# Optimization experiments

Measured on AMD Instinct MI355X. Metric: run time of the kernel, lower is better.

The kernel has to match this reference:

```python
import jax, jax.numpy as jnp
import numpy as np

N_USER = 150_000
M_ITEM = 30_000
N_NODES = N_USER + M_ITEM
D = 64                      # embedding_dim
N_LAYERS = 3                # gcn_layer_number
E = 600_000                 # user-item interactions (symmetric nnz = 2E)
B = 1024
NUM_RATE, NUM_GENRE, NUM_DIR, NUM_ACT = 6, 25, 2186, 8030
NUM_GENDER, NUM_AGE, NUM_OCC, NUM_ZIP = 2, 7, 21, 3402
H1, H2 = 64, 64             # first/second fc hidden dims
FC1_IN = D * 10


def setup_inputs() -> dict:
    key = jax.random.key(0)
    ks = jax.random.split(key, 24)
    # aux features: 0/1 values are valid indices for every categorical field
    aux_info = jax.random.randint(ks[0], (B, 10246), 0, 2, dtype=jnp.int32)
    user_ids = jax.random.randint(ks[1], (B,), 0, N_USER, dtype=jnp.int32)
    item_ids = jax.random.randint(ks[2], (B,), 0, M_ITEM, dtype=jnp.int32)
    # bipartite graph: random interactions, symmetric normalized adjacency
    u = jax.random.randint(ks[3], (E,), 0, N_USER, dtype=jnp.int32)
    i = jax.random.randint(ks[4], (E,), 0, M_ITEM, dtype=jnp.int32) + N_USER
    graph_row = jnp.concatenate([u, i])
    graph_col = jnpph = jnp.concatenate([i, u]) if False else jnp.concatenate([i, u])
    deg = jax.ops.segment_sum(jnp.ones((2 * E,), jnp.float32), graph_row, num_segments=N_NODES)
    dinv = jnp.where(deg > 0, jax.lax.rsqrt(jnp.maximum(deg, 1.0)), 0.0)
    graph_val = dinv[graph_row] * dinv[graph_col]
    s = 0.1
    nrm = lambda k, shp: (jax.random.normal(k, shp, jnp.float32) * s)
    return {
        "aux_info": aux_info, "user_ids": user_ids, "item_ids": item_ids,
        "graph_row": graph_row, "graph_col": graph_col, "graph_val": graph_val,
        "rate_tab": nrm(ks[5], (NUM_RATE, D)),
        "genre_W": nrm(ks[6], (NUM_GENRE, D)),
        "director_W": nrm(ks[7], (NUM_DIR, D)),
        "actor_W": nrm(ks[8], (NUM_ACT, D)),
        "gender_tab": nrm(ks[9], (NUM_GENDER, D)),
        "age_tab": nrm(ks[10], (NUM_AGE, D)),
        "occ_tab": nrm(ks[11], (NUM_OCC, D)),
        "area_tab": nrm(ks[12], (NUM_ZIP, D)),
        "user_rel": nrm(ks[13], (N_USER, D)),
        "item_rel": nrm(ks[14], (M_ITEM, D)),
        "fc1_W": nrm(ks[15], (FC1_IN, H1)), "fc1_b": jnp.zeros((H1,), jnp.float32),
        "fc2_W": nrm(ks[16], (H1, H2)), "fc2_b": jnp.zeros((H2,), jnp.float32),
        "out_W": nrm(ks[17], (H2, 1)), "out_b": jnp.zeros((1,), jnp.float32),
    }


def _lightgcn(user_rel, item_rel, row, col, val):
    # LightGCN: repeated SpMM D^-1/2 A D^-1/2 @ emb, mean over layer outputs
    emb = jnp.concatenate([user_rel, item_rel], axis=0)      # [N, D]
    acc = emb
    for _ in range(N_LAYERS):
        emb = jax.ops.segment_sum(val[:, None] * emb[col], row, num_segments=N_NODES)
        acc = acc + emb
    light = acc / (N_LAYERS + 1)
    return light[:N_USER], light[N_USER:]


def _multi_hot(idx_int, W):
    x = idx_int.astype(jnp.float32)
    return (x @ W) / jnp.sum(x, axis=1, keepdims=True)


def reference(aux_info, user_ids, item_ids, graph_row, graph_col, graph_val,
              rate_tab, genre_W, director_W, actor_W,
              gender_tab, age_tab, occ_tab, area_tab,
              user_rel, item_rel,
              fc1_W, fc1_b, fc2_W, fc2_b, out_W, out_b):
    rate_idx = aux_info[:, 0]
    genre_idx = aux_info[:, 1:26]
    director_idx = aux_info[:, 26:2212]
    actor_idx = aux_info[:, 2212:10242]
    gender_idx = aux_info[:, 10242]
    age_idx = aux_info[:, 10243]
    occ_idx = aux_info[:, 10244]
    area_idx = aux_info[:, 10245]

    item_emb = jnp.concatenate([
        rate_tab[rate_idx],
        _multi_hot(genre_idx, genre_W),
        _multi_hot(director_idx, director_W),
        _multi_hot(actor_idx, actor_W),
    ], axis=1)                                               # [B, 4D]
    user_emb = jnp.concatenate([
        gender_tab[gender_idx], age_tab[age_idx],
        occ_tab[occ_idx], area_tab[area_idx],
    ], axis=1)                                               # [B, 4D]

    all_users, all_items = _lightgcn(user_rel, item_rel, graph_row, graph_col, graph_val)
    X = jnp.concatenate([item_emb, user_emb,
                         all_users[user_ids], all_items[item_ids]], axis=1)  # [B, 10D]
    X = jax.nn.relu(X @ fc1_W + fc1_b)
    X = jax.nn.relu(X @ fc2_W + fc2_b)
    return X @ out_W + out_b                                 # [B, 1]
```

## Files before the change

kernel.cpp:

```cpp
#include <hip/hip_runtime.h>
#include <hip/hip_bf16.h>
#include <hip/hip_fp16.h>

#define N_USER 150000
#define M_ITEM 30000
#define N_NODES 180000
#define E2 1200000
#define BATCH 1024
#define AUX_W 10246
#define KP_G 32
#define KP_D 2208
#define KP_A 8064
#define NBKT 265
#define WT_BLKS 2576
#define BCNT_BLKS 293
#define MH_BLKS 672
#define CVT_BLKS 5625

typedef __attribute__((ext_vector_type(8))) short short8;
typedef __attribute__((ext_vector_type(8))) unsigned short ushort8_t;
typedef __attribute__((ext_vector_type(4))) float f32x4;

__device__ __forceinline__ int bucket_of(int r) {
    return r < N_USER ? (r >> 10) : 147 + ((r - N_USER) >> 8);
}

__device__ __forceinline__ int detect_f32(const void* probe) {
    float v = __bfloat162float(((const __hip_bfloat16*)probe)[threadIdx.x & 63]);
    unsigned long long m = __ballot(!(fabsf(v) < 1000.0f));
    return __popcll(m) > 8;
}

struct CvtSeg { const void* src; float* dst; int n; int blk0; };
struct CvtBatch { CvtSeg seg[16]; };

__global__ void __launch_bounds__(256) k_prep(CvtBatch cb, int cvtBlks,
                                              const void* Wg, const void* Wd, const void* Wa,
                                              unsigned short* WtG, unsigned short* WtD, unsigned short* WtA,
                                              const int* __restrict__ grow, int* __restrict__ bucket_tot,
                                              const void* probe) {
    int blk = blockIdx.x, tid = threadIdx.x;
    if (blk < BCNT_BLKS) {
        __shared__ int h[NBKT];
        for (int i = tid; i < NBKT; i += 256) h[i] = 0;
        __syncthreads();
        int idx0 = blk * 4096;
        #pragma unroll
        for (int k = 0; k < 16; ++k) {
            int i = idx0 + k * 256 + tid;
            if (i < E2) atomicAdd(&h[bucket_of(grow[i])], 1);
        }
        __syncthreads();
        for (int i = tid; i < NBKT; i += 256) if (h[i]) atomicAdd(&bucket_tot[i], h[i]);
        return;
    }
    if (blk < BCNT_BLKS + cvtBlks) {
        int isf32 = detect_f32(probe);
        int cblk = blk - BCNT_BLKS;
        int si = 0;
        #pragma unroll
        for (int i = 0; i < 16; ++i) if (cblk >= cb.seg[i].blk0) si = i;
        const CvtSeg sg = cb.seg[si];
        int i = (cblk - sg.blk0) * 256 + tid;
        if (i >= sg.n) return;
        if (isf32) sg.dst[i] = ((const float*)sg.src)[i];
        else       sg.dst[i] = __bfloat162float(((const __hip_bfloat16*)sg.src)[i]);
        return;
    }
    {
        int isf32 = detect_f32(probe);
        int t = (blk - BCNT_BLKS - cvtBlks) * 256 + tid;
        if (t >= (KP_G + KP_D + KP_A) * 64) return;
        int kp = t >> 6, n = t & 63;
        int k, K; const void* src; unsigned short* dst;
        if (kp < KP_G)              { k = kp;               K = 25;   src = Wg; dst = WtG; }
        else if (kp < KP_G + KP_D)  { k = kp - KP_G;        K = 2186; src = Wd; dst = WtD; }
        else                        { k = kp - KP_G - KP_D; K = 8030; src = Wa; dst = WtA; }
        unsigned short v = 0;
        if (k < K) {
            if (isf32) {
                __hip_bfloat16 h = __float2bfloat16(((const float*)src)[(size_t)k * 64 + n]);
                v = *(unsigned short*)&h;
            } else {
                v = ((const unsigned short*)src)[(size_t)k * 64 + n];
            }
        }
        dst[(((size_t)(k >> 5) * 64 + n) * 4 + ((k >> 3) & 3)) * 8 + (k & 7)] = v;
    }
}

__global__ void __launch_bounds__(512) k_bscan(const int* __restrict__ bucket_tot,
                                               int* __restrict__ bucket_base,
                                               int* __restrict__ bucketcur) {
    __shared__ int s[512];
    int tid = threadIdx.x;
    s[tid] = (tid < NBKT) ? bucket_tot[tid] : 0;
    __syncthreads();
    for (int off = 1; off < 512; off <<= 1) {
        int v = (tid >= off) ? s[tid - off] : 0;
        __syncthreads();
        s[tid] += v;
        __syncthreads();
    }
    int excl = tid ? s[tid - 1] : 0;
    bucket_base[tid] = excl;
    if (tid < NBKT) bucketcur[tid] = excl;
}

__device__ void mhgemm_body(int blk, const int* __restrict__ aux,
                            const unsigned short* __restrict__ WtG,
                            const unsigned short* __restrict__ WtD,
                            const unsigned short* __restrict__ WtA,
                            float* __restrict__ Xmh, float* __restrict__ cntf) {
    int seg, rb, k0, klen, Kseg, auxoff;
    const unsigned short* Wt;
    if (blk < 16)       { seg = 0; rb = blk;                      k0 = 0;              klen = 25;                  Kseg = 25;   auxoff = 1;    Wt = WtG; }
    else if (blk < 160) { int t = blk - 16;  seg = 1; rb = t & 15; k0 = (t >> 4) * 256; klen = min(256, 2186 - k0); Kseg = 2186; auxoff = 26;   Wt = WtD; }
    else                { int t = blk - 160; seg = 2; rb = t & 15; k0 = (t >> 4) * 256; klen = min(256, 8030 - k0); Kseg = 8030; auxoff = 2212; Wt = WtA; }
    int lane = threadIdx.x & 63, wave = threadIdx.x >> 6;
    int m = lane & 15, quad = lane >> 4;
    int row = rb * 64 + wave * 16 + m;
    const int* arow = aux + (size_t)row * AUX_W + auxoff;

    f32x4 acc0 = {0.f,0.f,0.f,0.f}, acc1 = acc0, acc2 = acc0, acc3 = acc0;
    int isum = 0;
    int nchunk = (klen + 31) >> 5;
    int pa[8], na[8];
    auto lda = [&](int kci, int (&A)[8]) {
        int kb = k0 + kci * 32 + quad * 8;
        if (kb + 8 <= Kseg) {
            #pragma unroll
            for (int j = 0; j < 8; ++j) A[j] = arow[kb + j];
        } else {
            #pragma unroll
            for (int j = 0; j < 8; ++j) A[j] = (kb + j < Kseg) ? arow[kb + j] : 0;
        }
    };
    lda(0, pa);
    for (int kci = 0; kci < nchunk; ++kci) {
        if (kci + 1 < nchunk) lda(kci + 1, na);
        union { unsigned u[4]; short8 s; } af;
        af.u[0] = (unsigned)pa[0] * 16256u + (unsigned)pa[1] * 0x3F800000u;
        af.u[1] = (unsigned)pa[2] * 16256u + (unsigned)pa[3] * 0x3F800000u;
        af.u[2] = (unsigned)pa[4] * 16256u + (unsigned)pa[5] * 0x3F800000u;
        af.u[3] = (unsigned)pa[6] * 16256u + (unsigned)pa[7] * 0x3F800000u;
        isum += pa[0] + pa[1] + pa[2] + pa[3] + pa[4] + pa[5] + pa[6] + pa[7];
        size_t kcg = (size_t)(k0 >> 5) + kci;
        const unsigned short* bp = Wt + ((kcg * 64 + m) * 4 + quad) * 8;
        short8 b0 = *(const short8*)(bp);
        short8 b1 = *(const short8*)(bp + 512);
        short8 b2 = *(const short8*)(bp + 1024);
        short8 b3 = *(const short8*)(bp + 1536);
        acc0 = __builtin_amdgcn_mfma_f32_16x16x32_bf16(af.s, b0, acc0, 0, 0, 0);
        acc1 = __builtin_amdgcn_mfma_f32_16x16x32_bf16(af.s, b1, acc1, 0, 0, 0);
        acc2 = __builtin_amdgcn_mfma_f32_16x16x32_bf16(af.s, b2, acc2, 0, 0, 0);
        acc3 = __builtin_amdgcn_mfma_f32_16x16x32_bf16(af.s, b3, acc3, 0, 0, 0);
        #pragma unroll
        for (int j = 0; j < 8; ++j) pa[j] = na[j];
    }
    float asum = (float)isum;
    asum += __shfl_xor(asum, 16);
    asum += __shfl_xor(asum, 32);
    if (quad == 0) atomicAdd(&cntf[seg * BATCH + row], asum);
    float* xbase = Xmh + ((size_t)seg * BATCH + rb * 64 + wave * 16 + quad * 4) * 64;
    #pragma unroll
    for (int reg = 0; reg < 4; ++reg) {
        float* xr = xbase + (size_t)reg * 64;
        atomicAdd(&xr[ 0 + m], acc0[reg]);
        atomicAdd(&xr[16 + m], acc1[reg]);
        atomicAdd(&xr[32 + m], acc2[reg]);
        atomicAdd(&xr[48 + m], acc3[reg]);
    }
}

__global__ void __launch_bounds__(256) k_p1(const int* __restrict__ grow, const int* __restrict__ gcol,
                                            int* __restrict__ bucketcur, int2* __restrict__ binned,
                                            const int* __restrict__ aux,
                                            const unsigned short* __restrict__ WtG,
                                            const unsigned short* __restrict__ WtD,
                                            const unsigned short* __restrict__ WtA,
                                            float* __restrict__ Xmh, float* __restrict__ cntf) {
    int blk = blockIdx.x;
    if (blk < MH_BLKS) {
        mhgemm_body(blk, aux, WtG, WtD, WtA, Xmh, cntf);
        return;
    }
    __shared__ int h1[NBKT], base1[NBKT];
    int tid = threadIdx.x;
    for (int i = tid; i < NBKT; i += 256) h1[i] = 0;
    __syncthreads();
    int idx0 = (blk - MH_BLKS) * 4096;
    int r[16], c[16];
    #pragma unroll
    for (int k = 0; k < 16; ++k) {
        int i = idx0 + k * 256 + tid;
        if (i < E2) {
            r[k] = grow[i]; c[k] = gcol[i];
            atomicAdd(&h1[bucket_of(r[k])], 1);
        } else r[k] = -1;
    }
    __syncthreads();
    for (int i = tid; i < NBKT; i += 256) {
        base1[i] = h1[i] ? atomicAdd(&bucketcur[i], h1[i]) : 0;
        h1[i] = 0;
    }
    __syncthreads();
    #pragma unroll
    for (int k = 0; k < 16; ++k) {
        if (r[k] >= 0) {
            int b = bucket_of(r[k]);
            int p = base1[b] + atomicAdd(&h1[b], 1);
            binned[p] = make_int2(r[k], c[k]);
        }
    }
}

__global__ void __launch_bounds__(256) k_p2(const int2* __restrict__ binned, const int* __restrict__ bb,
                                            int* __restrict__ cols, int2* __restrict__ moffs,
                                            float* __restrict__ dinv, float* __restrict__ dsq,
                                            float* __restrict__ gsc) {
    __shared__ int h[1024];
    __shared__ int ws2[256];
    int b = blockIdx.x, tid = threadIdx.x;
    int r0, r1;
    if (b < 147) { r0 = b << 10; r1 = min((b + 1) << 10, N_USER); }
    else         { r0 = N_USER + ((b - 147) << 8); r1 = min(N_USER + ((b - 146) << 8), N_NODES); }
    int s0 = bb[b], e0 = bb[b + 1];
    for (int i = tid; i < 1024; i += 256) h[i] = 0;
    __syncthreads();
    for (int j = s0 + tid; j < e0; j += 256) atomicAdd(&h[binned[j].x - r0], 1);
    __syncthreads();
    int t0 = tid * 4;
    int a0 = h[t0], a1 = h[t0 + 1], a2 = h[t0 + 2], a3 = h[t0 + 3];
    ws2[tid] = a0 + a1 + a2 + a3;
    __syncthreads();
    for (int off = 1; off < 256; off <<= 1) {
        int v = (tid >= off) ? ws2[tid - off] : 0;
        __syncthreads();
        ws2[tid] += v;
        __syncthreads();
    }
    int excl = tid ? ws2[tid - 1] : 0;
    int ex[4] = { excl, excl + a0, excl + a0 + a1, excl + a0 + a1 + a2 };
    int ac[4] = { a0, a1, a2, a3 };
    #pragma unroll
    for (int i = 0; i < 4; ++i) {
        int row = r0 + t0 + i;
        if (row < r1) {
            moffs[row] = make_int2(s0 + ex[i], s0 + ex[i] + ac[i]);
            float deg = (float)ac[i];
            bool nz = deg > 0.f;
            dinv[row] = nz ? rsqrtf(deg) : 0.f;
            dsq[row]  = nz ? 1.f / deg  : 0.f;
            gsc[row]  = nz ? sqrtf(deg) : 0.f;
        }
        h[t0 + i] = ex[i];
    }
    __syncthreads();
    for (int j = s0 + tid; j < e0; j += 256) {
        int2 e = binned[j];
        int p = s0 + atomicAdd(&h[e.x - r0], 1);
        cols[p] = e.y << 7;
    }
}

__global__ void __launch_bounds__(256) k_cvt(const void* rawU, const void* rawI,
                                             const float* __restrict__ dinv,
                                             __half* __restrict__ emb) {
    int isf32 = detect_f32(rawU);
    int q = blockIdx.x * 256 + threadIdx.x;
    if (q >= N_NODES * 8) return;
    int r = q >> 3;
    const void* src; size_t qq;
    if (r < N_USER) { src = rawU; qq = (size_t)q; }
    else            { src = rawI; qq = (size_t)q - (size_t)N_USER * 8; }
    float d = dinv[r];
    float f[8];
    if (isf32) {
        float4 a = ((const float4*)src)[qq * 2], b = ((const float4*)src)[qq * 2 + 1];
        f[0]=a.x; f[1]=a.y; f[2]=a.z; f[3]=a.w; f[4]=b.x; f[5]=b.y; f[6]=b.z; f[7]=b.w;
    } else {
        ushort8_t u = ((const ushort8_t*)src)[qq];
        #pragma unroll
        for (int i = 0; i < 8; ++i) {
            unsigned short us = u[i];
            f[i] = __bfloat162float(*(__hip_bfloat16*)&us);
        }
    }
    ushort8_t o;
    #pragma unroll
    for (int i = 0; i < 8; ++i) {
        __half h = __float2half(f[i] * d);
        o[i] = *(unsigned short*)&h;
    }
    ((ushort8_t*)emb)[(size_t)q] = o;
}

__global__ void __launch_bounds__(256, 8) k_spmv(const __half* __restrict__ src, __half* __restrict__ dst,
                                                 const int2* __restrict__ moffs_in, const int* __restrict__ cols,
                                                 const float* __restrict__ dsq,
                                                 int spmvN, float* __restrict__ tacc,
                                                 const int* __restrict__ uids, const int* __restrict__ iids,
                                                 const float* __restrict__ gsc,
                                                 const void* rawU, const void* rawI,
                                                 int2* __restrict__ moffs2, int xmode) {
    int tid = threadIdx.x, lane = tid & 63;
    int blk = blockIdx.x;
    if (blk >= spmvN) {
        if (xmode == 1) {
            int t = (blk - spmvN) * 4 + (tid >> 6);
            int r = (t < BATCH) ? uids[t] : (N_USER + iids[t - BATCH]);
            tacc[(size_t)t * 64 + lane] += __half2float(src[(size_t)r * 64 + lane]) * gsc[r];
            return;
        }
        if (blk < spmvN + 512) {
            int t = (blk - spmvN) * 4 + (tid >> 6);
            int r = (t < BATCH) ? uids[t] : (N_USER + iids[t - BATCH]);
            int2 se = moffs_in[r];
            if (lane == 0) moffs2[r] = se;
            for (int j = se.x + lane; j < se.y; j += 64) {
                int c = (unsigned)cols[j] >> 7;
                moffs2[c] = moffs_in[c];
            }
            return;
        }
        {
            int isf32 = detect_f32(rawU);
            int t = (blk - spmvN - 512) * 4 + (tid >> 6);
            const void* s; size_t ri;
            if (t < BATCH) { s = rawU; ri = (size_t)uids[t]; }
            else           { s = rawI; ri = (size_t)iids[t - BATCH]; }
            float v;
            if (isf32) v = ((const float*)s)[ri * 64 + lane];
            else       v = __bfloat162float(((const __hip_bfloat16*)s)[ri * 64 + lane]);
            tacc[(size_t)t * 64 + lane] = v;
            return;
        }
    }
    int wid8 = blk * 4 + (tid >> 6);
    int g = lane >> 3, l8 = lane & 7;
    int r = wid8 * 8 + g;
    int2 se = moffs_in[r];
    int s = se.x, e = se.y;
    const char* sb = (const char*)src + (l8 << 4);
    float2 a0 = {0.f,0.f}, a1 = a0, a2 = a0, a3 = a0;
    int j0 = s;
    for (; j0 + 4 <= e; j0 += 4) {
        int c[4];
        #pragma unroll
        for (int u = 0; u < 4; ++u) c[u] = cols[j0 + u];
        float4 rv[4];
        #pragma unroll
        for (int u = 0; u < 4; ++u) rv[u] = *(const float4*)(sb + (size_t)(unsigned)c[u]);
        #pragma unroll
        for (int u = 0; u < 4; ++u) {
            const __half2* h = (const __half2*)&rv[u];
            float2 f0 = __half22float2(h[0]), f1 = __half22float2(h[1]);
            float2 f2 = __half22float2(h[2]), f3 = __half22float2(h[3]);
            a0.x += f0.x; a0.y += f0.y; a1.x += f1.x; a1.y += f1.y;
            a2.x += f2.x; a2.y += f2.y; a3.x += f3.x; a3.y += f3.y;
        }
    }
    if (j0 < e) {
        int c[4]; float w[4];
        #pragma unroll
        for (int u = 0; u < 4; ++u) {
            int j = j0 + u;
            c[u] = cols[min(j, e - 1)];
            w[u] = (j < e) ? 1.f : 0.f;
        }
        float4 rv[4];
        #pragma unroll
        for (int u = 0; u < 4; ++u) rv[u] = *(const float4*)(sb + (size_t)(unsigned)c[u]);
        #pragma unroll
        for (int u = 0; u < 4; ++u) {
            const __half2* h = (const __half2*)&rv[u];
            float2 f0 = __half22float2(h[0]), f1 = __half22float2(h[1]);
            float2 f2 = __half22float2(h[2]), f3 = __half22float2(h[3]);
            a0.x = fmaf(w[u], f0.x, a0.x); a0.y = fmaf(w[u], f0.y, a0.y);
            a1.x = fmaf(w[u], f1.x, a1.x); a1.y = fmaf(w[u], f1.y, a1.y);
            a2.x = fmaf(w[u], f2.x, a2.x); a2.y = fmaf(w[u], f2.y, a2.y);
            a3.x = fmaf(w[u], f3.x, a3.x); a3.y = fmaf(w[u], f3.y, a3.y);
        }
    }
    if (e > s) {
        float d = dsq[r];
        float4 ov;
        __half2* op = (__half2*)&ov;
        op[0] = __floats2half2_rn(a0.x * d, a0.y * d);
        op[1] = __floats2half2_rn(a1.x * d, a1.y * d);
        op[2] = __floats2half2_rn(a2.x * d, a2.y * d);
        op[3] = __floats2half2_rn(a3.x * d, a3.y * d);
        *(float4*)((char*)dst + ((size_t)r << 7) + (l8 << 4)) = ov;
    }
}

__global__ void __launch_bounds__(256) k_spmv3(const __half* __restrict__ src, float* __restrict__ tacc,
                                               const int2* __restrict__ moffs, const int* __restrict__ cols,
                                               const float* __restrict__ dinv, const float* __restrict__ gsc,
                                               const int* __restrict__ uids, const int* __restrict__ iids) {
    int tid = threadIdx.x, lane = tid & 63;
    int t = blockIdx.x * 4 + (tid >> 6);
    if (t >= 2048) return;
    int r = (t < BATCH) ? uids[t] : (N_USER + iids[t - BATCH]);
    int2 se = moffs[r];
    int s = se.x, e = se.y;
    int p = lane & 31, ep = lane >> 5;
    const char* sb = (const char*)src + (p << 2);
    float ax = 0.f, ay = 0.f;
    int j0 = s;
    for (; j0 + 16 <= e; j0 += 16) {
        int c[8];
        #pragma unroll
        for (int u = 0; u < 8; ++u) c[u] = cols[j0 + 2 * u + ep];
        float2 v[8];
        #pragma unroll
        for (int u = 0; u < 8; ++u) v[u] = __half22float2(*(const __half2*)(sb + (size_t)(unsigned)c[u]));
        #pragma unroll
        for (int u = 0; u < 8; ++u) { ax += v[u].x; ay += v[u].y; }
    }
    if (j0 + 8 <= e) {
        int c[4];
        #pragma unroll
        for (int u = 0; u < 4; ++u) c[u] = cols[j0 + 2 * u + ep];
        float2 v[4];
        #pragma unroll
        for (int u = 0; u < 4; ++u) v[u] = __half22float2(*(const __half2*)(sb + (size_t)(unsigned)c[u]));
        #pragma unroll
        for (int u = 0; u < 4; ++u) { ax += v[u].x; ay += v[u].y; }
        j0 += 8;
    }
    if (j0 + 4 <= e) {
        int c0 = cols[j0 + ep], c1 = cols[j0 + 2 + ep];
        float2 v0 = __half22float2(*(const __half2*)(sb + (size_t)(unsigned)c0));
        float2 v1 = __half22float2(*(const __half2*)(sb + (size_t)(unsigned)c1));
        ax += v0.x + v1.x; ay += v0.y + v1.y;
        j0 += 4;
    }
    if (j0 < e) {
        int j1 = j0 + ep, j2 = j0 + 2 + ep;
        int c0 = cols[min(j1, e - 1)], c1 = cols[min(j2, e - 1)];
        float w0 = (j1 < e) ? 1.f : 0.f, w1 = (j2 < e) ? 1.f : 0.f;
        float2 v0 = __half22float2(*(const __half2*)(sb + (size_t)(unsigned)c0));
        float2 v1 = __half22float2(*(const __half2*)(sb + (size_t)(unsigned)c1));
        ax = fmaf(w0, v0.x, ax); ay = fmaf(w0, v0.y, ay);
        ax = fmaf(w1, v1.x, ax); ay = fmaf(w1, v1.y, ay);
    }
    ax += __shfl_xor(ax, 32);
    ay += __shfl_xor(ay, 32);
    if (ep == 0) {
        float2 self = __half22float2(*(const __half2*)((const char*)src + ((size_t)r << 7) + (p << 2)));
        float di = dinv[r], g = gsc[r];
        float* tp = tacc + (size_t)t * 64 + (p << 1);
        tp[0] += di * ax + g * self.x;
        tp[1] += di * ay + g * self.y;
    }
}

__global__ void __launch_bounds__(256) k_mlp(const int* __restrict__ aux,
                                             const float* __restrict__ ratef, const float* __restrict__ genderf,
                                             const float* __restrict__ agef, const float* __restrict__ occf,
                                             const float* __restrict__ areaf, const float* __restrict__ tacc,
                                             const float* __restrict__ Xmh, const float* __restrict__ cntf,
                                             const float* __restrict__ W1, const float* __restrict__ b1,
                                             const float* __restrict__ W2, const float* __restrict__ b2,
                                             const float* __restrict__ Wo, const float* __restrict__ bo,
                                             void* __restrict__ out, const void* probe) {
    __shared__ float sx[4][640];
    __shared__ float sh[4][64];
    int isf32 = detect_f32(probe);
    int lane = threadIdx.x & 63, w = threadIdx.x >> 6;
    int b = blockIdx.x * 4 + w;
    const int* arow = aux + (size_t)b * AUX_W;
    float* xr = sx[w];
    xr[0   + lane] = ratef[arow[0] * 64 + lane];
    xr[64  + lane] = Xmh[((size_t)0 * BATCH + b) * 64 + lane] / cntf[0 * BATCH + b];
    xr[128 + lane] = Xmh[((size_t)1 * BATCH + b) * 64 + lane] / cntf[1 * BATCH + b];
    xr[192 + lane] = Xmh[((size_t)2 * BATCH + b) * 64 + lane] / cntf[2 * BATCH + b];
    xr[256 + lane] = genderf[arow[10242] * 64 + lane];
    xr[320 + lane] = agef[arow[10243] * 64 + lane];
    xr[384 + lane] = occf[arow[10244] * 64 + lane];
    xr[448 + lane] = areaf[arow[10245] * 64 + lane];
    xr[512 + lane] = tacc[(size_t)b * 64 + lane] * 0.25f;
    xr[576 + lane] = tacc[(size_t)(BATCH + b) * 64 + lane] * 0.25f;
    float acc = b1[lane];
    #pragma unroll 8
    for (int k = 0; k < 640; ++k) acc += xr[k] * W1[(size_t)k * 64 + lane];
    float h1 = fmaxf(acc, 0.f);
    sh[w][lane] = h1;
    float acc2 = b2[lane];
    #pragma unroll 8
    for (int j = 0; j < 64; ++j) acc2 += sh[w][j] * W2[(size_t)j * 64 + lane];
    float h2 = fmaxf(acc2, 0.f);
    float p = h2 * Wo[lane];
    #pragma unroll
    for (int off = 32; off; off >>= 1) p += __shfl_down(p, off);
    if (lane == 0) {
        float r = p + bo[0];
        if (isf32) ((float*)out)[b] = r;
        else       ((__hip_bfloat16*)out)[b] = __float2bfloat16(r);
    }
}

extern "C" void kernel_launch(void* const* d_in, const int* in_sizes, int n_in,
                              void* d_out, int out_size, void* d_ws, size_t ws_size,
                              hipStream_t stream) {
    const int* aux  = (const int*)d_in[0];
    const int* uids = (const int*)d_in[1];
    const int* iids = (const int*)d_in[2];
    const int* grow = (const int*)d_in[3];
    const int* gcol = (const int*)d_in[4];

    char* p = (char*)d_ws;
    auto alloc = [&](size_t bytes) -> char* {
        char* r = p;
        p += (bytes + 255) / 256 * 256;
        return r;
    };
    int*   bucket_tot  = (int*)alloc(512 * 4);
    float* Xmh         = (float*)alloc((size_t)3 * BATCH * 64 * 4);
    float* cntf        = (float*)alloc((size_t)3 * BATCH * 4);
    int2*  moffs2      = (int2*)alloc((size_t)180224 * 8);
    char*  zero_end    = p;
    int*   bucket_base = (int*)alloc(512 * 4);
    int*   bucketcur   = (int*)alloc(512 * 4);
    int2*  moffs       = (int2*)alloc((size_t)180224 * 8);
    float* dinv        = (float*)alloc((size_t)180224 * 4);
    float* dsq         = (float*)alloc((size_t)180224 * 4);
    float* gsc         = (float*)alloc((size_t)180224 * 4);
    int2*  binned      = (int2*)alloc((size_t)E2 * 8);
    int*   cols        = (int*)alloc((size_t)E2 * 4);
    __half* embA       = (__half*)alloc((size_t)N_NODES * 64 * 2);
    __half* embB       = (__half*)alloc((size_t)N_NODES * 64 * 2);
    float* tacc        = (float*)alloc((size_t)2048 * 64 * 4);
    unsigned short* WtG = (unsigned short*)alloc((size_t)KP_G * 64 * 2);
    unsigned short* WtD = (unsigned short*)alloc((size_t)KP_D * 64 * 2);
    unsigned short* WtA = (unsigned short*)alloc((size_t)KP_A * 64 * 2);
    float* ratef   = (float*)alloc(384 * 4);
    float* genderf = (float*)alloc(128 * 4);
    float* agef    = (float*)alloc(448 * 4);
    float* occf    = (float*)alloc(1344 * 4);
    float* areaf   = (float*)alloc((size_t)217728 * 4);
    float* fc1W    = (float*)alloc((size_t)40960 * 4);
    float* fc1b    = (float*)alloc(64 * 4);
    float* fc2W    = (float*)alloc(4096 * 4);
    float* fc2b    = (float*)alloc(64 * 4);
    float* outW    = (float*)alloc(64 * 4);
    float* outb    = (float*)alloc(4);

    const void* probe = d_in[14];

    hipMemsetAsync(bucket_tot, 0, (size_t)(zero_end - (char*)bucket_tot), stream);

    CvtBatch cb;
    int blk = 0, si = 0;
    auto addseg = [&](const void* s, float* d, int n) {
        cb.seg[si].src = s; cb.seg[si].dst = d; cb.seg[si].n = n; cb.seg[si].blk0 = blk;
        blk += (n + 255) / 256; ++si;
    };
    addseg(d_in[6],  ratef,   384);
    addseg(d_in[10], genderf, 128);
    addseg(d_in[11], agef,    448);
    addseg(d_in[12], occf,    1344);
    addseg(d_in[13], areaf,   217728);
    addseg(d_in[16], fc1W,   40960);
    addseg(d_in[17], fc1b,   64);
    addseg(d_in[18], fc2W,   4096);
    addseg(d_in[19], fc2b,   64);
    addseg(d_in[20], outW,   64);
    addseg(d_in[21], outb,   1);
    for (int i = si; i < 16; ++i) { cb.seg[i].src = nullptr; cb.seg[i].dst = nullptr; cb.seg[i].n = 0; cb.seg[i].blk0 = 0x7fffffff; }
    const int cvtBlks = blk;
    hipLaunchKernelGGL(k_prep, dim3(BCNT_BLKS + cvtBlks + WT_BLKS), dim3(256), 0, stream,
                       cb, cvtBlks, d_in[7], d_in[8], d_in[9], WtG, WtD, WtA, grow, bucket_tot, probe);

    hipLaunchKernelGGL(k_bscan, dim3(1), dim3(512), 0, stream, bucket_tot, bucket_base, bucketcur);
    hipLaunchKernelGGL(k_p1, dim3(MH_BLKS + BCNT_BLKS), dim3(256), 0, stream,
                       grow, gcol, bucketcur, binned, aux, WtG, WtD, WtA, Xmh, cntf);
    hipLaunchKernelGGL(k_p2, dim3(NBKT), dim3(256), 0, stream, binned, bucket_base, cols, moffs, dinv, dsq, gsc);

    hipLaunchKernelGGL(k_cvt, dim3(CVT_BLKS), dim3(256), 0, stream,
                       d_in[14], d_in[15], dinv, embA);

    const int spmvN = N_NODES / 32;
    hipLaunchKernelGGL(k_spmv, dim3(spmvN + 1024), dim3(256), 0, stream,
                       embA, embB, moffs, cols, dsq, spmvN, tacc, uids, iids, gsc,
                       d_in[14], d_in[15], moffs2, 0);
    hipLaunchKernelGGL(k_spmv, dim3(spmvN + 512), dim3(256), 0, stream,
                       embB, embA, moffs2, cols, dsq, spmvN, tacc, uids, iids, gsc,
                       d_in[14], d_in[15], moffs2, 1);
    hipLaunchKernelGGL(k_spmv3, dim3(2048 / 4), dim3(256), 0, stream,
                       embA, tacc, moffs, cols, dinv, gsc, uids, iids);

    hipLaunchKernelGGL(k_mlp, dim3(BATCH / 4), dim3(256), 0, stream,
                       aux, ratef, genderf, agef, occf, areaf, tacc, Xmh, cntf,
                       fc1W, fc1b, fc2W, fc2b, outW, outb, d_out, probe);
}
```

Measured before the change: 290.4 us.

## Fuse embedding conversion into first SpMV and third layer into MLP kernel

Removes the k_cvt pass that scaled raw bf16/f32 embeddings by dinv into a half buffer. The first propagation layer now gathers raw embeddings directly and applies the per-neighbour dinv weight inline. The third-layer gather for the batch rows is folded into the MLP kernel, which drops the k_spmv3 launch. The trade-off is an extra dinv load per edge and wider raw rows in the f32 case, in exchange for skipping a full write and re-read of the 180k x 64 table and two launches.

```diff
diff --git a/kernel.cpp b/kernel.cpp
--- a/kernel.cpp
+++ b/kernel.cpp
@@ -15,7 +15,6 @@
 #define WT_BLKS 2576
 #define BCNT_BLKS 293
 #define MH_BLKS 672
-#define CVT_BLKS 5625
 
 typedef __attribute__((ext_vector_type(8))) short short8;
 typedef __attribute__((ext_vector_type(8))) unsigned short ushort8_t;
@@ -29,6 +28,11 @@
     float v = __bfloat162float(((const __hip_bfloat16*)probe)[threadIdx.x & 63]);
     unsigned long long m = __ballot(!(fabsf(v) < 1000.0f));
     return __popcll(m) > 8;
+}
+
+__device__ __forceinline__ float bf16_to_f32(unsigned short u) {
+    unsigned x = (unsigned)u << 16;
+    return *(float*)&x;
 }
 
 struct CvtSeg { const void* src; float* dst; int n; int blk0; };
@@ -264,55 +268,18 @@
     }
 }
 
-__global__ void __launch_bounds__(256) k_cvt(const void* rawU, const void* rawI,
-                                             const float* __restrict__ dinv,
-                                             __half* __restrict__ emb) {
-    int isf32 = detect_f32(rawU);
-    int q = blockIdx.x * 256 + threadIdx.x;
-    if (q >= N_NODES * 8) return;
-    int r = q >> 3;
-    const void* src; size_t qq;
-    if (r < N_USER) { src = rawU; qq = (size_t)q; }
-    else            { src = rawI; qq = (size_t)q - (size_t)N_USER * 8; }
-    float d = dinv[r];
-    float f[8];
-    if (isf32) {
-        float4 a = ((const float4*)src)[qq * 2], b = ((const float4*)src)[qq * 2 + 1];
-        f[0]=a.x; f[1]=a.y; f[2]=a.z; f[3]=a.w; f[4]=b.x; f[5]=b.y; f[6]=b.z; f[7]=b.w;
-    } else {
-        ushort8_t u = ((const ushort8_t*)src)[qq];
-        #pragma unroll
-        for (int i = 0; i < 8; ++i) {
-            unsigned short us = u[i];
-            f[i] = __bfloat162float(*(__hip_bfloat16*)&us);
-        }
-    }
-    ushort8_t o;
-    #pragma unroll
-    for (int i = 0; i < 8; ++i) {
-        __half h = __float2half(f[i] * d);
-        o[i] = *(unsigned short*)&h;
-    }
-    ((ushort8_t*)emb)[(size_t)q] = o;
-}
-
-__global__ void __launch_bounds__(256, 8) k_spmv(const __half* __restrict__ src, __half* __restrict__ dst,
-                                                 const int2* __restrict__ moffs_in, const int* __restrict__ cols,
-                                                 const float* __restrict__ dsq,
-                                                 int spmvN, float* __restrict__ tacc,
-                                                 const int* __restrict__ uids, const int* __restrict__ iids,
-                                                 const float* __restrict__ gsc,
-                                                 const void* rawU, const void* rawI,
-                                                 int2* __restrict__ moffs2, int xmode) {
+__global__ void __launch_bounds__(256, 8) k_spmv_raw(const void* rawU, const void* rawI,
+                                                     __half* __restrict__ dst,
+                                                     const int2* __restrict__ moffs_in,
+                                                     const int* __restrict__ cols,
+                                                     const float* __restrict__ dinv,
+                                                     const float* __restrict__ dsq,
+                                                     int spmvN, float* __restrict__ tacc,
+                                                     const int* __restrict__ uids, const int* __restrict__ iids,
+                                                     int2* __restrict__ moffs2) {
     int tid = threadIdx.x, lane = tid & 63;
     int blk = blockIdx.x;
     if (blk >= spmvN) {
-        if (xmode == 1) {
-            int t = (blk - spmvN) * 4 + (tid >> 6);
-            int r = (t < BATCH) ? uids[t] : (N_USER + iids[t - BATCH]);
-            tacc[(size_t)t * 64 + lane] += __half2float(src[(size_t)r * 64 + lane]) * gsc[r];
-            return;
-        }
         if (blk < spmvN + 512) {
             int t = (blk - spmvN) * 4 + (tid >> 6);
             int r = (t < BATCH) ? uids[t] : (N_USER + iids[t - BATCH]);
@@ -337,6 +304,106 @@
             return;
         }
     }
+    int isf32 = detect_f32(rawU);
+    int wid8 = blk * 4 + (tid >> 6);
+    int g = lane >> 3, l8 = lane & 7;
+    int r = wid8 * 8 + g;
+    int2 se = moffs_in[r];
+    int s = se.x, e = se.y;
+    float a[8] = {0.f,0.f,0.f,0.f,0.f,0.f,0.f,0.f};
+    int j0 = s;
+    if (!isf32) {
+        const char* nb = (r < N_USER) ? (const char*)rawI - ((size_t)N_USER << 7)
+                                      : (const char*)rawU;
+        const char* sb = nb + (l8 << 4);
+        for (; j0 + 4 <= e; j0 += 4) {
+            int c[4]; float w[4];
+            #pragma unroll
+            for (int u = 0; u < 4; ++u) { c[u] = cols[j0 + u]; w[u] = dinv[(unsigned)c[u] >> 7]; }
+            float4 rv[4];
+            #pragma unroll
+            for (int u = 0; u < 4; ++u) rv[u] = *(const float4*)(sb + (size_t)(unsigned)c[u]);
+            #pragma unroll
+            for (int u = 0; u < 4; ++u) {
+                const unsigned short* us = (const unsigned short*)&rv[u];
+                #pragma unroll
+                for (int k = 0; k < 8; ++k) a[k] = fmaf(w[u], bf16_to_f32(us[k]), a[k]);
+            }
+        }
+        if (j0 < e) {
+            int c[4]; float w[4];
+            #pragma unroll
+            for (int u = 0; u < 4; ++u) {
+                int j = j0 + u;
+                c[u] = cols[min(j, e - 1)];
+                w[u] = (j < e) ? dinv[(unsigned)c[u] >> 7] : 0.f;
+            }
+            float4 rv[4];
+            #pragma unroll
+            for (int u = 0; u < 4; ++u) rv[u] = *(const float4*)(sb + (size_t)(unsigned)c[u]);
+            #pragma unroll
+            for (int u = 0; u < 4; ++u) {
+                const unsigned short* us = (const unsigned short*)&rv[u];
+                #pragma unroll
+                for (int k = 0; k < 8; ++k) a[k] = fmaf(w[u], bf16_to_f32(us[k]), a[k]);
+            }
+        }
+    } else {
+        const char* nb = (r < N_USER) ? (const char*)rawI - ((size_t)N_USER << 8)
+                                      : (const char*)rawU;
+        const char* sb = nb + (l8 << 5);
+        for (; j0 + 2 <= e; j0 += 2) {
+            int c0 = cols[j0], c1 = cols[j0 + 1];
+            float w0 = dinv[(unsigned)c0 >> 7], w1 = dinv[(unsigned)c1 >> 7];
+            const char* p0 = sb + ((size_t)(unsigned)c0 << 1);
+            const char* p1 = sb + ((size_t)(unsigned)c1 << 1);
+            float4 v0a = *(const float4*)(p0), v0b = *(const float4*)(p0 + 16);
+            float4 v1a = *(const float4*)(p1), v1b = *(const float4*)(p1 + 16);
+            const float* f0 = (const float*)&v0a; const float* f0b = (const float*)&v0b;
+            const float* f1 = (const float*)&v1a; const float* f1b = (const float*)&v1b;
+            #pragma unroll
+            for (int k = 0; k < 4; ++k) { a[k] = fmaf(w0, f0[k], a[k]); a[4 + k] = fmaf(w0, f0b[k], a[4 + k]); }
+            #pragma unroll
+            for (int k = 0; k < 4; ++k) { a[k] = fmaf(w1, f1[k], a[k]); a[4 + k] = fmaf(w1, f1b[k], a[4 + k]); }
+        }
+        if (j0 < e) {
+            int c0 = cols[j0];
+            float w0 = dinv[(unsigned)c0 >> 7];
+            const char* p0 = sb + ((size_t)(unsigned)c0 << 1);
+            float4 v0a = *(const float4*)(p0), v0b = *(const float4*)(p0 + 16);
+            const float* f0 = (const float*)&v0a; const float* f0b = (const float*)&v0b;
+            #pragma unroll
+            for (int k = 0; k < 4; ++k) { a[k] = fmaf(w0, f0[k], a[k]); a[4 + k] = fmaf(w0, f0b[k], a[4 + k]); }
+        }
+    }
+    if (e > s) {
+        float d = dsq[r];
+        float4 ov;
+        __half2* op = (__half2*)&ov;
+        op[0] = __floats2half2_rn(a[0] * d, a[1] * d);
+        op[1] = __floats2half2_rn(a[2] * d, a[3] * d);
+        op[2] = __floats2half2_rn(a[4] * d, a[5] * d);
+        op[3] = __floats2half2_rn(a[6] * d, a[7] * d);
+        *(float4*)((char*)dst + ((size_t)r << 7) + (l8 << 4)) = ov;
+    }
+}
+
+__global__ void __launch_bounds__(256, 8) k_spmv(const __half* __restrict__ src, __half* __restrict__ dst,
+                                                 const int2* __restrict__ moffs_in, const int* __restrict__ cols,
+                                                 const float* __restrict__ dsq,
+                                                 int spmvN, float* __restrict__ tacc,
+                                                 const int* __restrict__ uids, const int* __restrict__ iids,
+                                                 const float* __restrict__ gsc) {
+    int tid = threadIdx.x, lane = tid & 63;
+    int blk = blockIdx.x;
+    if (blk >= spmvN) {
+        int t = (blk - spmvN) * 4 + (tid >> 6);
+        int r = (t < BATCH) ? uids[t] : (N_USER + iids[t - BATCH]);
+        float g = gsc[r];
+        float h = __half2float(src[(size_t)r * 64 + lane]);
+        tacc[(size_t)t * 64 + lane] += (g > 0.f) ? h * g : 0.f;
+        return;
+    }
     int wid8 = blk * 4 + (tid >> 6);
     int g = lane >> 3, l8 = lane & 7;
     int r = wid8 * 8 + g;
@@ -395,68 +462,6 @@
     }
 }
 
-__global__ void __launch_bounds__(256) k_spmv3(const __half* __restrict__ src, float* __restrict__ tacc,
-                                               const int2* __restrict__ moffs, const int* __restrict__ cols,
-                                               const float* __restrict__ dinv, const float* __restrict__ gsc,
-                                               const int* __restrict__ uids, const int* __restrict__ iids) {
-    int tid = threadIdx.x, lane = tid & 63;
-    int t = blockIdx.x * 4 + (tid >> 6);
-    if (t >= 2048) return;
-    int r = (t < BATCH) ? uids[t] : (N_USER + iids[t - BATCH]);
-    int2 se = moffs[r];
-    int s = se.x, e = se.y;
-    int p = lane & 31, ep = lane >> 5;
-    const char* sb = (const char*)src + (p << 2);
-    float ax = 0.f, ay = 0.f;
-    int j0 = s;
-    for (; j0 + 16 <= e; j0 += 16) {
-        int c[8];
-        #pragma unroll
-        for (int u = 0; u < 8; ++u) c[u] = cols[j0 + 2 * u + ep];
-        float2 v[8];
-        #pragma unroll
-        for (int u = 0; u < 8; ++u) v[u] = __half22float2(*(const __half2*)(sb + (size_t)(unsigned)c[u]));
-        #pragma unroll
-        for (int u = 0; u < 8; ++u) { ax += v[u].x; ay += v[u].y; }
-    }
-    if (j0 + 8 <= e) {
-        int c[4];
-        #pragma unroll
-        for (int u = 0; u < 4; ++u) c[u] = cols[j0 + 2 * u + ep];
-        float2 v[4];
-        #pragma unroll
-        for (int u = 0; u < 4; ++u) v[u] = __half22float2(*(const __half2*)(sb + (size_t)(unsigned)c[u]));
-        #pragma unroll
-        for (int u = 0; u < 4; ++u) { ax += v[u].x; ay += v[u].y; }
-        j0 += 8;
-    }
-    if (j0 + 4 <= e) {
-        int c0 = cols[j0 + ep], c1 = cols[j0 + 2 + ep];
-        float2 v0 = __half22float2(*(const __half2*)(sb + (size_t)(unsigned)c0));
-        float2 v1 = __half22float2(*(const __half2*)(sb + (size_t)(unsigned)c1));
-        ax += v0.x + v1.x; ay += v0.y + v1.y;
-        j0 += 4;
-    }
-    if (j0 < e) {
-        int j1 = j0 + ep, j2 = j0 + 2 + ep;
-        int c0 = cols[min(j1, e - 1)], c1 = cols[min(j2, e - 1)];
-        float w0 = (j1 < e) ? 1.f : 0.f, w1 = (j2 < e) ? 1.f : 0.f;
-        float2 v0 = __half22float2(*(const __half2*)(sb + (size_t)(unsigned)c0));
-        float2 v1 = __half22float2(*(const __half2*)(sb + (size_t)(unsigned)c1));
-        ax = fmaf(w0, v0.x, ax); ay = fmaf(w0, v0.y, ay);
-        ax = fmaf(w1, v1.x, ax); ay = fmaf(w1, v1.y, ay);
-    }
-    ax += __shfl_xor(ax, 32);
-    ay += __shfl_xor(ay, 32);
-    if (ep == 0) {
-        float2 self = __half22float2(*(const __half2*)((const char*)src + ((size_t)r << 7) + (p << 2)));
-        float di = dinv[r], g = gsc[r];
-        float* tp = tacc + (size_t)t * 64 + (p << 1);
-        tp[0] += di * ax + g * self.x;
-        tp[1] += di * ay + g * self.y;
-    }
-}
-
 __global__ void __launch_bounds__(256) k_mlp(const int* __restrict__ aux,
                                              const float* __restrict__ ratef, const float* __restrict__ genderf,
                                              const float* __restrict__ agef, const float* __restrict__ occf,
@@ -465,7 +470,11 @@
                                              const float* __restrict__ W1, const float* __restrict__ b1,
                                              const float* __restrict__ W2, const float* __restrict__ b2,
                                              const float* __restrict__ Wo, const float* __restrict__ bo,
-                                             void* __restrict__ out, const void* probe) {
+                                             void* __restrict__ out, const void* probe,
+                                             const __half* __restrict__ embA,
+                                             const int2* __restrict__ moffs, const int* __restrict__ cols,
+                                             const float* __restrict__ dinv, const float* __restrict__ gsc,
+                                             const int* __restrict__ uids, const int* __restrict__ iids) {
     __shared__ float sx[4][640];
     __shared__ float sh[4][64];
     int isf32 = detect_f32(probe);
@@ -473,6 +482,70 @@
     int b = blockIdx.x * 4 + w;
     const int* arow = aux + (size_t)b * AUX_W;
     float* xr = sx[w];
+
+    #pragma unroll 1
+    for (int which = 0; which < 2; ++which) {
+        int t = which ? (BATCH + b) : b;
+        int r = which ? (N_USER + iids[b]) : uids[b];
+        int2 se = moffs[r];
+        int s = se.x, e = se.y;
+        int p = lane & 31, ep = lane >> 5;
+        const char* sb = (const char*)embA + (p << 2);
+        float ax = 0.f, ay = 0.f;
+        int j0 = s;
+        for (; j0 + 16 <= e; j0 += 16) {
+            int c[8];
+            #pragma unroll
+            for (int u = 0; u < 8; ++u) c[u] = cols[j0 + 2 * u + ep];
+            float2 v[8];
+            #pragma unroll
+            for (int u = 0; u < 8; ++u) v[u] = __half22float2(*(const __half2*)(sb + (size_t)(unsigned)c[u]));
+            #pragma unroll
+            for (int u = 0; u < 8; ++u) { ax += v[u].x; ay += v[u].y; }
+        }
+        if (j0 + 8 <= e) {
+            int c[4];
+            #pragma unroll
+            for (int u = 0; u < 4; ++u) c[u] = cols[j0 + 2 * u + ep];
+            float2 v[4];
+            #pragma unroll
+            for (int u = 0; u < 4; ++u) v[u] = __half22float2(*(const __half2*)(sb + (size_t)(unsigned)c[u]));
+            #pragma unroll
+            for (int u = 0; u < 4; ++u) { ax += v[u].x; ay += v[u].y; }
+            j0 += 8;
+        }
+        if (j0 + 4 <= e) {
+            int c0 = cols[j0 + ep], c1 = cols[j0 + 2 + ep];
+            float2 v0 = __half22float2(*(const __half2*)(sb + (size_t)(unsigned)c0));
+            float2 v1 = __half22float2(*(const __half2*)(sb + (size_t)(unsigned)c1));
+            ax += v0.x + v1.x; ay += v0.y + v1.y;
+            j0 += 4;
+        }
+        if (j0 < e) {
+            int j1 = j0 + ep, j2 = j0 + 2 + ep;
+            int c0 = cols[min(j1, e - 1)], c1 = cols[min(j2, e - 1)];
+            float w0 = (j1 < e) ? 1.f : 0.f, w1 = (j2 < e) ? 1.f : 0.f;
+            float2 v0 = __half22float2(*(const __half2*)(sb + (size_t)(unsigned)c0));
+            float2 v1 = __half22float2(*(const __half2*)(sb + (size_t)(unsigned)c1));
+            ax = fmaf(w0, v0.x, ax); ay = fmaf(w0, v0.y, ay);
+            ax = fmaf(w1, v1.x, ax); ay = fmaf(w1, v1.y, ay);
+        }
+        ax += __shfl_xor(ax, 32);
+        ay += __shfl_xor(ay, 32);
+        if (ep == 0) {
+            float s0 = tacc[(size_t)t * 64 + (p << 1)];
+            float s1 = tacc[(size_t)t * 64 + (p << 1) + 1];
+            if (e > s) {
+                float2 self = __half22float2(*(const __half2*)((const char*)embA + ((size_t)r << 7) + (p << 2)));
+                float di = dinv[r], g = gsc[r];
+                s0 += di * ax + g * self.x;
+                s1 += di * ay + g * self.y;
+            }
+            xr[512 + (which << 6) + (p << 1)]     = s0 * 0.25f;
+            xr[512 + (which << 6) + (p << 1) + 1] = s1 * 0.25f;
+        }
+    }
+
     xr[0   + lane] = ratef[arow[0] * 64 + lane];
     xr[64  + lane] = Xmh[((size_t)0 * BATCH + b) * 64 + lane] / cntf[0 * BATCH + b];
     xr[128 + lane] = Xmh[((size_t)1 * BATCH + b) * 64 + lane] / cntf[1 * BATCH + b];
@@ -481,8 +554,6 @@
     xr[320 + lane] = agef[arow[10243] * 64 + lane];
     xr[384 + lane] = occf[arow[10244] * 64 + lane];
     xr[448 + lane] = areaf[arow[10245] * 64 + lane];
-    xr[512 + lane] = tacc[(size_t)b * 64 + lane] * 0.25f;
-    xr[576 + lane] = tacc[(size_t)(BATCH + b) * 64 + lane] * 0.25f;
     float acc = b1[lane];
     #pragma unroll 8
     for (int k = 0; k < 640; ++k) acc += xr[k] * W1[(size_t)k * 64 + lane];
@@ -579,20 +650,15 @@
                        grow, gcol, bucketcur, binned, aux, WtG, WtD, WtA, Xmh, cntf);
     hipLaunchKernelGGL(k_p2, dim3(NBKT), dim3(256), 0, stream, binned, bucket_base, cols, moffs, dinv, dsq, gsc);
 
-    hipLaunchKernelGGL(k_cvt, dim3(CVT_BLKS), dim3(256), 0, stream,
-                       d_in[14], d_in[15], dinv, embA);
-
     const int spmvN = N_NODES / 32;
-    hipLaunchKernelGGL(k_spmv, dim3(spmvN + 1024), dim3(256), 0, stream,
-                       embA, embB, moffs, cols, dsq, spmvN, tacc, uids, iids, gsc,
-                       d_in[14], d_in[15], moffs2, 0);
+    hipLaunchKernelGGL(k_spmv_raw, dim3(spmvN + 1024), dim3(256), 0, stream,
+                       d_in[14], d_in[15], embB, moffs, cols, dinv, dsq, spmvN,
+                       tacc, uids, iids, moffs2);
     hipLaunchKernelGGL(k_spmv, dim3(spmvN + 512), dim3(256), 0, stream,
-                       embB, embA, moffs2, cols, dsq, spmvN, tacc, uids, iids, gsc,
-                       d_in[14], d_in[15], moffs2, 1);
-    hipLaunchKernelGGL(k_spmv3, dim3(2048 / 4), dim3(256), 0, stream,
-                       embA, tacc, moffs, cols, dinv, gsc, uids, iids);
+                       embB, embA, moffs2, cols, dsq, spmvN, tacc, uids, iids, gsc);
 
     hipLaunchKernelGGL(k_mlp, dim3(BATCH / 4), dim3(256), 0, stream,
                        aux, ratef, genderf, agef, occf, areaf, tacc, Xmh, cntf,
-                       fc1W, fc1b, fc2W, fc2b, outW, outb, d_out, probe);
-}
+                       fc1W, fc1b, fc2W, fc2b, outW, outb, d_out, probe,
+                       embA, moffs, cols, dinv, gsc, uids, iids);
+}
```

Result: slower. 303.9 us (+4.7%).
